# Optimization experiments

Measured on AMD Instinct MI355X. Metric: run time of the kernel, lower is better.

## Reference

```python
import jax, jax.numpy as jnp
import numpy as np

B, C, H, W = 8, 256, 64, 64   # C = in_channels(64) * no_g(4)
DQK = 8                        # max(in_channels//8, no_g) = max(8,4)


def setup_inputs() -> dict:
    key = jax.random.key(0)
    ks = jax.random.split(key, 8)
    s_in = 1.0 / np.sqrt(C)
    return {
        "x": jax.random.normal(ks[0], (B, C, H, W), dtype=jnp.float32),
        "wq": jax.random.normal(ks[1], (DQK, C), dtype=jnp.float32) * s_in,
        "bq": jax.random.normal(ks[2], (DQK,), dtype=jnp.float32) * 0.01,
        "wk": jax.random.normal(ks[3], (DQK, C), dtype=jnp.float32) * s_in,
        "bk": jax.random.normal(ks[4], (DQK,), dtype=jnp.float32) * 0.01,
        "wv": jax.random.normal(ks[5], (C, C), dtype=jnp.float32) * s_in,
        "bv": jax.random.normal(ks[6], (C,), dtype=jnp.float32) * 0.01,
        "gamma": jax.random.normal(ks[7], (1,), dtype=jnp.float32) * 0.5,
    }


def reference(x, wq, bq, wk, bk, wv, bv, gamma):
    b, c, h, w = x.shape
    n = h * w
    xf = x.reshape(b, c, n)                                   # B,C,N
    q = (jnp.einsum('bcn,qc->bqn', xf, wq) + bq[None, :, None])  # B,DQK,N (1x1 conv)
    k = (jnp.einsum('bcn,qc->bqn', xf, wk) + bk[None, :, None])  # B,DQK,N
    v = (jnp.einsum('bcn,oc->bon', xf, wv) + bv[None, :, None])  # B,C,N
    energy = jnp.einsum('bdn,bdm->bnm', q, k)                 # B,N,N (no scale, as in source)
    attn = jax.nn.softmax(energy, axis=-1)                    # softmax over last dim
    # out[b,c,m] = sum_n v[b,c,n] * attn[b,m,n]  (bmm(V, A^T))
    out = jnp.einsum('bcn,bmn->bcm', v, attn).reshape(b, c, h, w)
    return gamma[0] * out + x
```

## Files before the change

kernel.cpp:

```cpp
#include <hip/hip_runtime.h>
#include <math.h>

namespace {

constexpr int B_ = 8;
constexpr int C_ = 256;
constexpr int N_ = 4096;

constexpr int TM = 64;
constexpr int TN = 128;
constexpr int NCH = N_ / TN;
constexpr int PSTRIDE = 136;
constexpr float LOG2E = 1.4426950408889634f;

constexpr int VBLK = C_ * 16;

typedef __attribute__((ext_vector_type(8))) short short8;
typedef __attribute__((ext_vector_type(16))) float float16;

__device__ inline unsigned short f2bf(float f) {
  unsigned u = __float_as_uint(f);
  u += 0x7FFFu + ((u >> 16) & 1u);
  return (unsigned short)(u >> 16);
}
__device__ inline float bf2f(unsigned short h) {
  return __uint_as_float(((unsigned)h) << 16);
}

__device__ inline float fast_exp2(float x) {
  float r;
  asm("v_exp_f32 %0, %1" : "=v"(r) : "v"(x));
  return r;
}

__global__ __launch_bounds__(256) void prep_kernel(
    const float* __restrict__ wv, const float* __restrict__ wq,
    const float* __restrict__ wk,
    unsigned short* __restrict__ wv_bf, unsigned short* __restrict__ wqk_bf) {
  const int i = blockIdx.x * 256 + threadIdx.x;
  wv_bf[i] = f2bf(wv[i]);
  if (i < 2048) {
    const int d = i >> 8, c = i & 255;
    const float qL = wq[i] * LOG2E;
    const unsigned short hq = f2bf(qL);
    wqk_bf[d * 256 + c]        = hq;
    wqk_bf[(d + 8) * 256 + c]  = f2bf(qL - bf2f(hq));
    const float kv = wk[i];
    const unsigned short hk = f2bf(kv);
    wqk_bf[(d + 16) * 256 + c] = hk;
    wqk_bf[(d + 24) * 256 + c] = f2bf(kv - bf2f(hk));
  }
}

__device__ inline short8 xfrag(const float* xs, int c0, int n) {
  const float* base = xs + c0 * 32 + n;
  uint4 p;
  asm("v_cvt_pk_bf16_f32 %0, %1, %2" : "=v"(p.x) : "v"(base[0]),   "v"(base[32]));
  asm("v_cvt_pk_bf16_f32 %0, %1, %2" : "=v"(p.y) : "v"(base[64]),  "v"(base[96]));
  asm("v_cvt_pk_bf16_f32 %0, %1, %2" : "=v"(p.z) : "v"(base[128]), "v"(base[160]));
  asm("v_cvt_pk_bf16_f32 %0, %1, %2" : "=v"(p.w) : "v"(base[192]), "v"(base[224]));
  return __builtin_bit_cast(short8, p);
}

__global__ __launch_bounds__(256, 4) void proj_kernel(
    const float* __restrict__ x,
    const float* __restrict__ bq, const float* __restrict__ bk,
    const unsigned short* __restrict__ wqk_bf,
    const unsigned short* __restrict__ wv_bf, const float* __restrict__ bv,
    unsigned short* __restrict__ q_t, unsigned short* __restrict__ k_th,
    unsigned short* __restrict__ k_tl, unsigned short* __restrict__ v)
{
  __shared__ float xs[256 * 32];

  const int b = blockIdx.y;
  const int n0 = blockIdx.x * 32;
  const int tid = threadIdx.x;
  const int w = tid >> 6, l = tid & 63;
  const int l31 = l & 31, lh = l >> 5;

  {
    const int r8 = l >> 3, c4 = (l & 7) * 4;
    const float* gp = x + ((size_t)b * C_ + w * 64 + r8) * N_ + n0 + c4;
    #pragma unroll
    for (int i = 0; i < 64; i += 8) {
      __builtin_amdgcn_global_load_lds(
          (const __attribute__((address_space(1))) void*)(gp + (size_t)i * N_),
          (__attribute__((address_space(3))) void*)(xs + (w * 64 + i) * 32), 16, 0, 0);
    }
  }
  __syncthreads();

  if (w == 0) {
    float16 sacc;
    #pragma unroll
    for (int r = 0; r < 16; ++r) sacc[r] = 0.f;
    for (int ks = 0; ks < 16; ++ks) {
      const short8 a = *reinterpret_cast<const short8*>(
          wqk_bf + l31 * 256 + ks * 16 + lh * 8);
      const short8 bfg = xfrag(xs, ks * 16 + lh * 8, l31);
      sacc = __builtin_amdgcn_mfma_f32_32x32x16_bf16(a, bfg, sacc, 0, 0, 0);
    }
    const size_t gn = (size_t)b * N_ + n0 + l31;
    #pragma unroll
    for (int r = 0; r < 4; ++r) {
      const int d = r + 4 * lh;
      const float qv = sacc[r] + sacc[r + 4] + bq[d] * LOG2E;
      const unsigned short hq = f2bf(qv);
      q_t[gn * 16 + d]     = hq;
      q_t[gn * 16 + 8 + d] = f2bf(qv - bf2f(hq));
      const float kv = sacc[r + 8] + sacc[r + 12] + bk[d];
      const unsigned short hk = f2bf(kv);
      k_th[gn * 8 + d] = hk;
      k_tl[gn * 8 + d] = f2bf(kv - bf2f(hk));
    }
  }

  float16 acc[2];
  #pragma unroll
  for (int mi = 0; mi < 2; ++mi)
    #pragma unroll
    for (int r = 0; r < 16; ++r) acc[mi][r] = 0.f;

  for (int ks = 0; ks < 16; ++ks) {
    short8 af[2];
    #pragma unroll
    for (int mi = 0; mi < 2; ++mi)
      af[mi] = *reinterpret_cast<const short8*>(
          wv_bf + (w * 64 + mi * 32 + l31) * C_ + ks * 16 + lh * 8);
    const short8 bfg = xfrag(xs, ks * 16 + lh * 8, l31);
    #pragma unroll
    for (int mi = 0; mi < 2; ++mi)
      acc[mi] = __builtin_amdgcn_mfma_f32_32x32x16_bf16(af[mi], bfg, acc[mi], 0, 0, 0);
  }

  const int p32 = (l31 & 3) | (((l31 >> 3) & 3) << 2) | (((l31 >> 2) & 1) << 4);
  const int P32 = n0 + p32;
  const int nblk = P32 >> 4, nin = P32 & 15;
  #pragma unroll
  for (int mi = 0; mi < 2; ++mi)
    #pragma unroll
    for (int r = 0; r < 16; ++r) {
      const int c = w * 64 + mi * 32 + (r & 3) + 8 * (r >> 2) + 4 * lh;
      v[(((size_t)b * (N_ / 16) + nblk) * C_ + c) * 16 + nin] =
          f2bf(acc[mi][r] + bv[c]);
    }
}

__global__ __launch_bounds__(256, 2) void attn_kernel(
    const unsigned short* __restrict__ q_t, const unsigned short* __restrict__ k_th,
    const unsigned short* __restrict__ k_tl, const unsigned short* __restrict__ v,
    const float* __restrict__ x, const float* __restrict__ gamma,
    float* __restrict__ out)
{
  __shared__ __align__(16) unsigned short ps[2][TM][PSTRIDE];
  __shared__ float rsp[4][TM];
  __shared__ float rsn[TM];

  const int b = blockIdx.x;
  const int m0 = blockIdx.y * TM;
  const int tid = threadIdx.x;
  const int w = tid >> 6;
  const int l = tid & 63;
  const int l31 = l & 31, lh = l >> 5;
  const int nrow = w * 32 + l31;

  const size_t qoff0 = ((size_t)b * N_ + m0 + l31) * 16;
  const short8 qh0 = *reinterpret_cast<const short8*>(q_t + qoff0);
  const short8 ql0 = *reinterpret_cast<const short8*>(q_t + qoff0 + 8);
  const short8 qh1 = *reinterpret_cast<const short8*>(q_t + qoff0 + 512);
  const short8 ql1 = *reinterpret_cast<const short8*>(q_t + qoff0 + 520);

  const unsigned short* kb = (lh ? k_tl : k_th) + (size_t)b * N_ * 8;

  const unsigned short* vlane0 =
      v + ((size_t)b * (N_ / 16)) * VBLK + (size_t)(2 * w * 32 + l31) * 16 + lh * 8;
  const unsigned short* vlane1 = vlane0 + 512;

  float16 o00, o01, o10, o11;
  #pragma unroll
  for (int r = 0; r < 16; ++r) { o00[r] = 0.f; o01[r] = 0.f; o10[r] = 0.f; o11[r] = 0.f; }
  float rsum0 = 0.f, rsum1 = 0.f;

  auto qk_tile = [&](const short8& kf, const short8& qh, const short8& ql,
                     float& rs, unsigned short* prow) {
    float16 s;
    #pragma unroll
    for (int r = 0; r < 16; ++r) s[r] = 0.f;
    s = __builtin_amdgcn_mfma_f32_32x32x16_bf16(kf, qh, s, 0, 0, 0);
    s = __builtin_amdgcn_mfma_f32_32x32x16_bf16(kf, ql, s, 0, 0, 0);
    float e[16];
    #pragma unroll
    for (int r = 0; r < 16; ++r) e[r] = fast_exp2(s[r]);
    rs += (((e[0] + e[1]) + (e[2] + e[3])) + ((e[4] + e[5]) + (e[6] + e[7]))) +
          (((e[8] + e[9]) + (e[10] + e[11])) + ((e[12] + e[13]) + (e[14] + e[15])));
    uint4 pk0, pk1;
    asm("v_cvt_pk_bf16_f32 %0, %1, %2" : "=v"(pk0.x) : "v"(e[0]), "v"(e[1]));
    asm("v_cvt_pk_bf16_f32 %0, %1, %2" : "=v"(pk0.y) : "v"(e[2]), "v"(e[3]));
    asm("v_cvt_pk_bf16_f32 %0, %1, %2" : "=v"(pk0.z) : "v"(e[4]), "v"(e[5]));
    asm("v_cvt_pk_bf16_f32 %0, %1, %2" : "=v"(pk0.w) : "v"(e[6]), "v"(e[7]));
    asm("v_cvt_pk_bf16_f32 %0, %1, %2" : "=v"(pk1.x) : "v"(e[8]), "v"(e[9]));
    asm("v_cvt_pk_bf16_f32 %0, %1, %2" : "=v"(pk1.y) : "v"(e[10]), "v"(e[11]));
    asm("v_cvt_pk_bf16_f32 %0, %1, %2" : "=v"(pk1.z) : "v"(e[12]), "v"(e[13]));
    asm("v_cvt_pk_bf16_f32 %0, %1, %2" : "=v"(pk1.w) : "v"(e[14]), "v"(e[15]));
    *reinterpret_cast<uint4*>(prow) = pk0;
    *reinterpret_cast<uint4*>(prow + 8) = pk1;
  };

  short8 af0[8], af1[8];
  #pragma unroll
  for (int g = 0; g < 8; ++g) {
    af0[g] = *reinterpret_cast<const short8*>(vlane0 + (size_t)g * VBLK);
    af1[g] = *reinterpret_cast<const short8*>(vlane1 + (size_t)g * VBLK);
  }
  short8 kf1 = *reinterpret_cast<const short8*>(kb + (size_t)(TN + nrow) * 8);
  {
    const short8 kf0 = *reinterpret_cast<const short8*>(kb + (size_t)nrow * 8);
    qk_tile(kf0, qh0, ql0, rsum0, &ps[0][l31][w * 32 + lh * 16]);
    qk_tile(kf0, qh1, ql1, rsum1, &ps[0][32 + l31][w * 32 + lh * 16]);
  }
  __syncthreads();

  for (int nc = 0; nc < NCH; ++nc) {
    const int buf = nc & 1;
    const bool more = (nc + 1) < NCH;
    const int nc1 = more ? (nc + 1) : 0;
    const int n2 = ((nc + 2) < NCH ? (nc + 2) : 0) * TN;

    const short8 kf2 = *reinterpret_cast<const short8*>(kb + (size_t)(n2 + nrow) * 8);

    if (more) {
      qk_tile(kf1, qh0, ql0, rsum0, &ps[buf ^ 1][l31][w * 32 + lh * 16]);
      qk_tile(kf1, qh1, ql1, rsum1, &ps[buf ^ 1][32 + l31][w * 32 + lh * 16]);
    }

    __builtin_amdgcn_s_setprio(1);
    #pragma unroll
    for (int ks = 0; ks < 8; ++ks) {
      const short8 p0 = *reinterpret_cast<const short8*>(&ps[buf][l31][ks * 16 + lh * 8]);
      const short8 p1 = *reinterpret_cast<const short8*>(&ps[buf][32 + l31][ks * 16 + lh * 8]);
      o00 = __builtin_amdgcn_mfma_f32_32x32x16_bf16(af0[ks], p0, o00, 0, 0, 0);
      o01 = __builtin_amdgcn_mfma_f32_32x32x16_bf16(af0[ks], p1, o01, 0, 0, 0);
      o10 = __builtin_amdgcn_mfma_f32_32x32x16_bf16(af1[ks], p0, o10, 0, 0, 0);
      o11 = __builtin_amdgcn_mfma_f32_32x32x16_bf16(af1[ks], p1, o11, 0, 0, 0);
      af0[ks] = *reinterpret_cast<const short8*>(vlane0 + (size_t)(nc1 * 8 + ks) * VBLK);
      af1[ks] = *reinterpret_cast<const short8*>(vlane1 + (size_t)(nc1 * 8 + ks) * VBLK);
    }
    __builtin_amdgcn_s_setprio(0);

    kf1 = kf2;
    __syncthreads();
  }

  rsum0 += __shfl_xor(rsum0, 32);
  rsum1 += __shfl_xor(rsum1, 32);
  if (l < 32) { rsp[w][l31] = rsum0; rsp[w][32 + l31] = rsum1; }
  __syncthreads();
  if (tid < TM) rsn[tid] = rsp[0][tid] + rsp[1][tid] + rsp[2][tid] + rsp[3][tid];
  __syncthreads();

  const float g = gamma[0];
  const float t0 = g / rsn[l31];
  const float t1 = g / rsn[32 + l31];
  #pragma unroll
  for (int r = 0; r < 16; ++r) {
    const int crow = (r & 3) + 8 * (r >> 2) + 4 * lh;
    const int c0 = 2 * w * 32 + crow;
    const size_t i00 = ((size_t)b * C_ + c0) * N_ + m0 + l31;
    const size_t i10 = i00 + (size_t)32 * N_;
    out[i00]      = fmaf(o00[r], t0, x[i00]);
    out[i00 + 32] = fmaf(o01[r], t1, x[i00 + 32]);
    out[i10]      = fmaf(o10[r], t0, x[i10]);
    out[i10 + 32] = fmaf(o11[r], t1, x[i10 + 32]);
  }
}

}

extern "C" void kernel_launch(void* const* d_in, const int* in_sizes, int n_in,
                              void* d_out, int out_size, void* d_ws, size_t ws_size,
                              hipStream_t stream) {
  const float* x     = (const float*)d_in[0];
  const float* wq    = (const float*)d_in[1];
  const float* bq    = (const float*)d_in[2];
  const float* wk    = (const float*)d_in[3];
  const float* bk    = (const float*)d_in[4];
  const float* wv    = (const float*)d_in[5];
  const float* bv    = (const float*)d_in[6];
  const float* gamma = (const float*)d_in[7];
  float* out = (float*)d_out;

  char* p = (char*)d_ws;
  unsigned short* q_t    = (unsigned short*)p;  p += (size_t)B_ * N_ * 16 * 2;
  unsigned short* k_th   = (unsigned short*)p;  p += (size_t)B_ * N_ * 8 * 2;
  unsigned short* k_tl   = (unsigned short*)p;  p += (size_t)B_ * N_ * 8 * 2;
  unsigned short* wv_bf  = (unsigned short*)p;  p += (size_t)C_ * C_ * 2;
  unsigned short* wqk_bf = (unsigned short*)p;  p += (size_t)32 * C_ * 2;
  unsigned short* v      = (unsigned short*)p;

  prep_kernel<<<dim3(C_ * C_ / 256), 256, 0, stream>>>(wv, wq, wk, wv_bf, wqk_bf);
  proj_kernel<<<dim3(N_ / 32, B_), 256, 0, stream>>>(x, bq, bk, wqk_bf, wv_bf, bv,
                                                     q_t, k_th, k_tl, v);
  attn_kernel<<<dim3(B_, N_ / TM), 256, 0, stream>>>(q_t, k_th, k_tl, v, x, gamma, out);
}
```

Baseline: 192.0 us.

## Split attention block across 8 waves, one 32-row query tile per wave

The attention kernel goes from 4 waves (256 threads) to 8 waves (512 threads) per block. Each wave now handles a single 32-row query tile against a 64-channel slice, so it keeps two accumulators instead of four. This halves per-wave register pressure and aims for more waves in flight to hide exp, LDS and memory latency. In exchange, each wave reloads the V fragments, since V is now fetched twice per block (once per query-tile half), and the block-wide barriers span more waves.

```diff
diff --git a/kernel.cpp b/kernel.cpp
--- a/kernel.cpp
+++ b/kernel.cpp
@@ -146,7 +146,7 @@
     }
 }
 
-__global__ __launch_bounds__(256, 2) void attn_kernel(
+__global__ __launch_bounds__(512, 4) void attn_kernel(
     const unsigned short* __restrict__ q_t, const unsigned short* __restrict__ k_th,
     const unsigned short* __restrict__ k_tl, const unsigned short* __restrict__ v,
     const float* __restrict__ x, const float* __restrict__ gamma,
@@ -162,27 +162,27 @@
   const int w = tid >> 6;
   const int l = tid & 63;
   const int l31 = l & 31, lh = l >> 5;
-  const int nrow = w * 32 + l31;
-
-  const size_t qoff0 = ((size_t)b * N_ + m0 + l31) * 16;
-  const short8 qh0 = *reinterpret_cast<const short8*>(q_t + qoff0);
-  const short8 ql0 = *reinterpret_cast<const short8*>(q_t + qoff0 + 8);
-  const short8 qh1 = *reinterpret_cast<const short8*>(q_t + qoff0 + 512);
-  const short8 ql1 = *reinterpret_cast<const short8*>(q_t + qoff0 + 520);
+  const int mt = w >> 2;
+  const int q  = w & 3;
+  const int nrow = q * 32 + l31;
+  const int mrow = mt * 32 + l31;
+
+  const size_t qoff = ((size_t)b * N_ + m0 + mrow) * 16;
+  const short8 qh = *reinterpret_cast<const short8*>(q_t + qoff);
+  const short8 ql = *reinterpret_cast<const short8*>(q_t + qoff + 8);
 
   const unsigned short* kb = (lh ? k_tl : k_th) + (size_t)b * N_ * 8;
 
   const unsigned short* vlane0 =
-      v + ((size_t)b * (N_ / 16)) * VBLK + (size_t)(2 * w * 32 + l31) * 16 + lh * 8;
+      v + ((size_t)b * (N_ / 16)) * VBLK + (size_t)(q * 64 + l31) * 16 + lh * 8;
   const unsigned short* vlane1 = vlane0 + 512;
 
-  float16 o00, o01, o10, o11;
-  #pragma unroll
-  for (int r = 0; r < 16; ++r) { o00[r] = 0.f; o01[r] = 0.f; o10[r] = 0.f; o11[r] = 0.f; }
-  float rsum0 = 0.f, rsum1 = 0.f;
-
-  auto qk_tile = [&](const short8& kf, const short8& qh, const short8& ql,
-                     float& rs, unsigned short* prow) {
+  float16 o0, o1;
+  #pragma unroll
+  for (int r = 0; r < 16; ++r) { o0[r] = 0.f; o1[r] = 0.f; }
+  float rsum = 0.f;
+
+  auto qk_tile = [&](const short8& kf, unsigned short* prow) {
     float16 s;
     #pragma unroll
     for (int r = 0; r < 16; ++r) s[r] = 0.f;
@@ -191,8 +191,8 @@
     float e[16];
     #pragma unroll
     for (int r = 0; r < 16; ++r) e[r] = fast_exp2(s[r]);
-    rs += (((e[0] + e[1]) + (e[2] + e[3])) + ((e[4] + e[5]) + (e[6] + e[7]))) +
-          (((e[8] + e[9]) + (e[10] + e[11])) + ((e[12] + e[13]) + (e[14] + e[15])));
+    rsum += (((e[0] + e[1]) + (e[2] + e[3])) + ((e[4] + e[5]) + (e[6] + e[7]))) +
+            (((e[8] + e[9]) + (e[10] + e[11])) + ((e[12] + e[13]) + (e[14] + e[15])));
     uint4 pk0, pk1;
     asm("v_cvt_pk_bf16_f32 %0, %1, %2" : "=v"(pk0.x) : "v"(e[0]), "v"(e[1]));
     asm("v_cvt_pk_bf16_f32 %0, %1, %2" : "=v"(pk0.y) : "v"(e[2]), "v"(e[3]));
@@ -215,8 +215,7 @@
   short8 kf1 = *reinterpret_cast<const short8*>(kb + (size_t)(TN + nrow) * 8);
   {
     const short8 kf0 = *reinterpret_cast<const short8*>(kb + (size_t)nrow * 8);
-    qk_tile(kf0, qh0, ql0, rsum0, &ps[0][l31][w * 32 + lh * 16]);
-    qk_tile(kf0, qh1, ql1, rsum1, &ps[0][32 + l31][w * 32 + lh * 16]);
+    qk_tile(kf0, &ps[0][mrow][q * 32 + lh * 16]);
   }
   __syncthreads();
 
@@ -229,19 +228,15 @@
     const short8 kf2 = *reinterpret_cast<const short8*>(kb + (size_t)(n2 + nrow) * 8);
 
     if (more) {
-      qk_tile(kf1, qh0, ql0, rsum0, &ps[buf ^ 1][l31][w * 32 + lh * 16]);
-      qk_tile(kf1, qh1, ql1, rsum1, &ps[buf ^ 1][32 + l31][w * 32 + lh * 16]);
+      qk_tile(kf1, &ps[buf ^ 1][mrow][q * 32 + lh * 16]);
     }
 
     __builtin_amdgcn_s_setprio(1);
     #pragma unroll
     for (int ks = 0; ks < 8; ++ks) {
-      const short8 p0 = *reinterpret_cast<const short8*>(&ps[buf][l31][ks * 16 + lh * 8]);
-      const short8 p1 = *reinterpret_cast<const short8*>(&ps[buf][32 + l31][ks * 16 + lh * 8]);
-      o00 = __builtin_amdgcn_mfma_f32_32x32x16_bf16(af0[ks], p0, o00, 0, 0, 0);
-      o01 = __builtin_amdgcn_mfma_f32_32x32x16_bf16(af0[ks], p1, o01, 0, 0, 0);
-      o10 = __builtin_amdgcn_mfma_f32_32x32x16_bf16(af1[ks], p0, o10, 0, 0, 0);
-      o11 = __builtin_amdgcn_mfma_f32_32x32x16_bf16(af1[ks], p1, o11, 0, 0, 0);
+      const short8 pm = *reinterpret_cast<const short8*>(&ps[buf][mrow][ks * 16 + lh * 8]);
+      o0 = __builtin_amdgcn_mfma_f32_32x32x16_bf16(af0[ks], pm, o0, 0, 0, 0);
+      o1 = __builtin_amdgcn_mfma_f32_32x32x16_bf16(af1[ks], pm, o1, 0, 0, 0);
       af0[ks] = *reinterpret_cast<const short8*>(vlane0 + (size_t)(nc1 * 8 + ks) * VBLK);
       af1[ks] = *reinterpret_cast<const short8*>(vlane1 + (size_t)(nc1 * 8 + ks) * VBLK);
     }
@@ -251,26 +246,22 @@
     __syncthreads();
   }
 
-  rsum0 += __shfl_xor(rsum0, 32);
-  rsum1 += __shfl_xor(rsum1, 32);
-  if (l < 32) { rsp[w][l31] = rsum0; rsp[w][32 + l31] = rsum1; }
+  rsum += __shfl_xor(rsum, 32);
+  if (l < 32) rsp[q][mrow] = rsum;
   __syncthreads();
   if (tid < TM) rsn[tid] = rsp[0][tid] + rsp[1][tid] + rsp[2][tid] + rsp[3][tid];
   __syncthreads();
 
   const float g = gamma[0];
-  const float t0 = g / rsn[l31];
-  const float t1 = g / rsn[32 + l31];
+  const float t = g / rsn[mrow];
   #pragma unroll
   for (int r = 0; r < 16; ++r) {
     const int crow = (r & 3) + 8 * (r >> 2) + 4 * lh;
-    const int c0 = 2 * w * 32 + crow;
-    const size_t i00 = ((size_t)b * C_ + c0) * N_ + m0 + l31;
-    const size_t i10 = i00 + (size_t)32 * N_;
-    out[i00]      = fmaf(o00[r], t0, x[i00]);
-    out[i00 + 32] = fmaf(o01[r], t1, x[i00 + 32]);
-    out[i10]      = fmaf(o10[r], t0, x[i10]);
-    out[i10 + 32] = fmaf(o11[r], t1, x[i10 + 32]);
+    const int c0 = q * 64 + crow;
+    const size_t i0 = ((size_t)b * C_ + c0) * N_ + m0 + mrow;
+    const size_t i1 = i0 + (size_t)32 * N_;
+    out[i0] = fmaf(o0[r], t, x[i0]);
+    out[i1] = fmaf(o1[r], t, x[i1]);
   }
 }
 
@@ -300,5 +291,5 @@
   prep_kernel<<<dim3(C_ * C_ / 256), 256, 0, stream>>>(wv, wq, wk, wv_bf, wqk_bf);
   proj_kernel<<<dim3(N_ / 32, B_), 256, 0, stream>>>(x, bq, bk, wqk_bf, wv_bf, bv,
                                                      q_t, k_th, k_tl, v);
-  attn_kernel<<<dim3(B_, N_ / TM), 256, 0, stream>>>(q_t, k_th, k_tl, v, x, gamma, out);
-}
+  attn_kernel<<<dim3(B_, N_ / TM), 512, 0, stream>>>(q_t, k_th, k_tl, v, x, gamma, out);
+}
```

New measurement: 296.4 us. 54.4% more time.
